# Optimization experiments

Measured on AMD Instinct MI355X. Metric: run time of the kernel, lower is better.

Reference implementation:

```python
import jax, jax.numpy as jnp
import numpy as np

BT, H, V = 4096, 2048, 32000
IGNORE_INDEX = -100


def setup_inputs() -> dict:
    key = jax.random.key(0)
    k1, k2, k3 = jax.random.split(key, 3)
    x = jax.random.normal(k1, (BT, H), dtype=jnp.float32)
    weight = jax.random.normal(k2, (V, H), dtype=jnp.float32) * 0.02
    target = jax.random.randint(k3, (BT,), 0, V, dtype=jnp.int64)
    return {"x": x, "weight": weight, "target": target}


def reference(x, weight, target):
    # logits: [BT, V] = x @ weight.T, accumulated in fp32 (as hl.dot out_dtype)
    logits = jnp.einsum("bh,vh->bv", x, weight).astype(jnp.float32)
    lse = jax.nn.logsumexp(logits, axis=-1)  # [BT]
    # picked target logit (target == ignore_index never matches any class,
    # matching the kernel's mask = (target[:,None] == vocab_offset))
    valid = target != IGNORE_INDEX
    safe_t = jnp.where(valid, target, 0)
    picked = jnp.take_along_axis(logits, safe_t[:, None], axis=-1)[:, 0]
    picked = jnp.where(valid, picked, 0.0)
    nll = lse - picked  # [BT]
    # reduction == 'mean': divide per-token nll by n_non_ignore, then sum
    n_non_ignore = valid.sum().astype(jnp.float32)
    loss = (nll / n_non_ignore).sum()
    return loss
```

## Files before the change

kernel.cpp:

```cpp
#include <hip/hip_runtime.h>
#include <hip/hip_bf16.h>

#define BT 4096
#define HD 2048
#define VD 32000
#define IGNORE_IDX (-100)

#define BM2 256
#define BN2 256
#define BK2 64
#define NRB2 (BT / BM2)
#define NCB2 (VD / BN2)
#define NKT (HD / BK2)

#define BM 128
#define BN 128
#define BKT 32
#define NRB (BT / BM)
#define NCB (VD / BN)

using short8 = __attribute__((ext_vector_type(8))) short;
using f32x4 = __attribute__((ext_vector_type(4))) float;
using i32x4 = __attribute__((ext_vector_type(4))) int;

__device__ __forceinline__ unsigned short f2bf(float f) {
  unsigned u = __float_as_uint(f);
  u = (u + 0x7fffu + ((u >> 16) & 1u)) >> 16;
  return (unsigned short)u;
}

#define GL(SRC, DST)                                         \
  __builtin_amdgcn_global_load_lds(                          \
      (const __attribute__((address_space(1))) void*)(SRC),  \
      (__attribute__((address_space(3))) void*)(DST), 16, 0, 0)

#define STG1(GSRC, KOFF, DBASE, SLOT) GL((GSRC) + (KOFF), (DBASE) + (SLOT)*8192)

__global__ void detect_tgt_kernel(const long long* __restrict__ t64,
                                  int* __restrict__ badcnt) {
  int i = blockIdx.x * blockDim.x + threadIdx.x;
  long long v = t64[i];
  bool valid = (v == (long long)IGNORE_IDX) || (v >= 0 && v < (long long)VD);
  if (!valid) atomicAdd(badcnt, 1);
}

__global__ __launch_bounds__(256) void quant_rows_kernel(
    const float* __restrict__ in, signed char* __restrict__ outq,
    float* __restrict__ scale) {
  const int row = blockIdx.x;
  const int t = threadIdx.x;
  const float* src = in + (size_t)row * HD;
  float4 v0 = ((const float4*)src)[2 * t];
  float4 v1 = ((const float4*)src)[2 * t + 1];
  float vv[8] = {v0.x, v0.y, v0.z, v0.w, v1.x, v1.y, v1.z, v1.w};
  float amax = 0.f;
#pragma unroll
  for (int i = 0; i < 8; i++) amax = fmaxf(amax, fabsf(vv[i]));
#pragma unroll
  for (int m = 1; m < 64; m <<= 1) amax = fmaxf(amax, __shfl_xor(amax, m, 64));
  __shared__ float wm4[4];
  if ((t & 63) == 0) wm4[t >> 6] = amax;
  __syncthreads();
  float am = fmaxf(fmaxf(wm4[0], wm4[1]), fmaxf(wm4[2], wm4[3]));
  float inv = am > 0.f ? 127.f / am : 0.f;
  if (t == 0) scale[row] = am > 0.f ? am / 127.f : 0.f;
  int lo = 0, hi = 0;
#pragma unroll
  for (int i = 0; i < 4; i++) {
    float f = fminf(fmaxf(vv[i] * inv, -127.f), 127.f);
    lo |= (__float2int_rn(f) & 0xff) << (8 * i);
  }
#pragma unroll
  for (int i = 0; i < 4; i++) {
    float f = fminf(fmaxf(vv[4 + i] * inv, -127.f), 127.f);
    hi |= (__float2int_rn(f) & 0xff) << (8 * i);
  }
  int2 pk = make_int2(lo, hi);
  *(int2*)(outq + (size_t)row * HD + t * 8) = pk;
}

__global__ __launch_bounds__(512, 2) void gemm_lse_i8_kernel(
    const signed char* __restrict__ xq, const signed char* __restrict__ wq,
    const float* __restrict__ sx, const float* __restrict__ sw,
    const void* __restrict__ tgt, const int* __restrict__ badcnt,
    float* __restrict__ partialS, float* __restrict__ picked) {
  __shared__ signed char smem[65536];
  signed char* ldsA = smem;
  signed char* ldsB = smem + 32768;

  const int t = threadIdx.x;

  {
    uint4 z = make_uint4(0u, 0u, 0u, 0u);
#pragma unroll
    for (int i = 0; i < 8; i++) ((uint4*)smem)[t + i * 512] = z;
  }
  __syncthreads();

  const int bid = blockIdx.x;
  const int cpx = (NRB2 * NCB2) >> 3;
  const int swz = (bid & 7) * cpx + (bid >> 3);
  const int rb = swz % NRB2;
  const int cb = swz / NRB2;
  const int row0 = rb * BM2;
  const int col0 = cb * BN2;

  const int lane = t & 63;
  const int w = t >> 6;
  const int wm = w >> 2;
  const int wn = w & 3;
  const int bh = wn >> 1;
  const int bn4 = wn & 1;

  const int fr = lane & 15;
  const int kq = lane >> 4;

  const signed char* pA0 = ldsA + (0 * 2 + wm) * 8192 + lane * 16;
  const signed char* pA1 = ldsA + (1 * 2 + wm) * 8192 + lane * 16;
  const signed char* pB0 = ldsB + (0 * 2 + bh) * 8192 + bn4 * 4096 + lane * 16;
  const signed char* pB1 = ldsB + (1 * 2 + bh) * 8192 + bn4 * 4096 + lane * 16;

  const int srow = lane & 15;
  const int scol = (lane >> 4) * 16;
  const signed char* gA0 = xq + (size_t)(row0 + 0 + w * 16 + srow) * HD + scol;
  const signed char* gA1 =
      xq + (size_t)(row0 + 128 + w * 16 + srow) * HD + scol;
  const signed char* gB0 = wq + (size_t)(col0 + 0 + w * 16 + srow) * HD + scol;
  const signed char* gB1 =
      wq + (size_t)(col0 + 128 + w * 16 + srow) * HD + scol;

  signed char* dA = ldsA + w * 1024;
  signed char* dB = ldsB + w * 1024;

  i32x4 acc[8][4];
#pragma unroll
  for (int i = 0; i < 8; i++)
#pragma unroll
    for (int n = 0; n < 4; n++)
#pragma unroll
      for (int q = 0; q < 4; q++) acc[i][n][q] = 0;

  i32x4 aLo[4], aHi[4], bLo[2], bHi[2];

#define RDALO(P)                                       \
  _Pragma("unroll") for (int i = 0; i < 4; i++)        \
      aLo[i] = *(const i32x4*)((P) + i * 1024);

#define RDAHI(P)                                       \
  _Pragma("unroll") for (int i = 0; i < 4; i++)        \
      aHi[i] = *(const i32x4*)((P) + (i + 4) * 1024);

#define RDB(P)                                         \
  _Pragma("unroll") for (int n = 0; n < 2; n++)        \
      bLo[n] = *(const i32x4*)((P) + n * 1024);        \
  _Pragma("unroll") for (int n = 0; n < 2; n++)        \
      bHi[n] = *(const i32x4*)((P) + (n + 2) * 1024);

#define MM_P1()                                                            \
  _Pragma("unroll") for (int i = 0; i < 4; i++) {                          \
    _Pragma("unroll") for (int n = 0; n < 2; n++)                          \
        acc[i][n] = __builtin_amdgcn_mfma_i32_16x16x64_i8(                 \
            aLo[i], bLo[n], acc[i][n], 0, 0, 0);                           \
    _Pragma("unroll") for (int n = 0; n < 2; n++)                          \
        acc[i][2 + n] = __builtin_amdgcn_mfma_i32_16x16x64_i8(             \
            aLo[i], bHi[n], acc[i][2 + n], 0, 0, 0);                       \
  }

#define MM_P2()                                                            \
  _Pragma("unroll") for (int i = 0; i < 4; i++)                            \
  _Pragma("unroll") for (int n = 0; n < 2; n++)                            \
      acc[4 + i][n] = __builtin_amdgcn_mfma_i32_16x16x64_i8(               \
          aHi[i], bLo[n], acc[4 + i][n], 0, 0, 0);

#define MM_P3()                                                            \
  _Pragma("unroll") for (int i = 0; i < 4; i++)                            \
  _Pragma("unroll") for (int n = 0; n < 2; n++)                            \
      acc[4 + i][2 + n] = __builtin_amdgcn_mfma_i32_16x16x64_i8(           \
          aHi[i], bHi[n], acc[4 + i][2 + n], 0, 0, 0);

#define PHASE(BODY)                                    \
  __builtin_amdgcn_sched_barrier(0);                   \
  __builtin_amdgcn_s_barrier();                        \
  asm volatile("s_waitcnt lgkmcnt(0)" ::: "memory");   \
  __builtin_amdgcn_sched_barrier(0);                   \
  __builtin_amdgcn_s_setprio(1);                       \
  BODY();                                              \
  __builtin_amdgcn_s_setprio(0);                       \
  __builtin_amdgcn_sched_barrier(0);                   \
  __builtin_amdgcn_s_barrier();                        \
  __builtin_amdgcn_sched_barrier(0);

  STG1(gA0, 0, dA, 0);
  STG1(gA1, 0, dA, 1);
  STG1(gB0, 0, dB, 0);
  STG1(gB1, 0, dB, 1);
  STG1(gB0, 64, dB, 2);
  STG1(gA0, 64, dA, 2);
  STG1(gA1, 64, dA, 3);
  asm volatile("s_waitcnt vmcnt(3)" ::: "memory");
  __builtin_amdgcn_s_barrier();

  for (int kt = 0; kt + 3 < NKT; kt += 2) {
    RDALO(pA0);
    RDB(pB0);
    STG1(gB1, 64, dB, 3);
    PHASE(MM_P1);
    RDAHI(pA0);
    STG1(gB0, 128, dB, 0);
    PHASE(MM_P2);
    STG1(gA0, 128, dA, 0);
    STG1(gA1, 128, dA, 1);
    asm volatile("s_waitcnt vmcnt(3)" ::: "memory");
    PHASE(MM_P3);
    RDALO(pA1);
    RDB(pB1);
    STG1(gB1, 128, dB, 1);
    PHASE(MM_P1);
    RDAHI(pA1);
    STG1(gB0, 192, dB, 2);
    PHASE(MM_P2);
    STG1(gA0, 192, dA, 2);
    STG1(gA1, 192, dA, 3);
    asm volatile("s_waitcnt vmcnt(3)" ::: "memory");
    PHASE(MM_P3);
    gA0 += 128;
    gA1 += 128;
    gB0 += 128;
    gB1 += 128;
  }

  {
    RDALO(pA0);
    RDB(pB0);
    STG1(gB1, 64, dB, 3);
    PHASE(MM_P1);
    RDAHI(pA0);
    PHASE(MM_P2);
    asm volatile("s_waitcnt vmcnt(0)" ::: "memory");
    PHASE(MM_P3);
    RDALO(pA1);
    RDB(pB1);
    PHASE(MM_P1);
    RDAHI(pA1);
    PHASE(MM_P2);
    PHASE(MM_P3);
  }

  __syncthreads();
  float* sxl = (float*)smem;
  float* swl = ((float*)smem) + 256;
  if (t < 256) {
    sxl[t] = sx[row0 + t];
    swl[t] = sw[col0 + t];
  }
  __syncthreads();
  float* red = ((float*)smem) + 512;
#pragma unroll
  for (int i = 0; i < 8; i++) {
#pragma unroll
    for (int q = 0; q < 4; q++) {
      int lrow = wm * 128 + i * 16 + kq * 4 + q;
      float sxr = sxl[lrow];
      float s = 0.f;
#pragma unroll
      for (int n = 0; n < 4; n++) {
        int lcol = wn * 64 + n * 16 + fr;
        s += __expf((float)acc[i][n][q] * sxr * swl[lcol]);
      }
#pragma unroll
      for (int m = 1; m < 16; m <<= 1) s += __shfl_xor(s, m, 64);
      if (fr == 0) red[lrow * 4 + wn] = s;
    }
  }
  __syncthreads();
  if (t < 256) {
    float S = red[t * 4 + 0] + red[t * 4 + 1] + red[t * 4 + 2] + red[t * 4 + 3];
    partialS[(size_t)cb * BT + row0 + t] = S;
  }

  const bool is64 = (*badcnt == 0);
#pragma unroll
  for (int i = 0; i < 8; i++) {
#pragma unroll
    for (int q = 0; q < 4; q++) {
      int lrow = wm * 128 + i * 16 + kq * 4 + q;
      int grow = row0 + lrow;
      long long tv = is64 ? ((const long long*)tgt)[grow]
                          : (long long)((const int*)tgt)[grow];
#pragma unroll
      for (int n = 0; n < 4; n++) {
        int lcol = wn * 64 + n * 16 + fr;
        int gcol = col0 + lcol;
        if (tv == (long long)gcol)
          picked[grow] = (float)acc[i][n][q] * sxl[lrow] * swl[lcol];
      }
    }
  }
#undef RDALO
#undef RDAHI
#undef RDB
#undef MM_P1
#undef MM_P2
#undef MM_P3
#undef PHASE
}

__global__ __launch_bounds__(256) void gemm_lse_kernel(
    const float* __restrict__ x, const float* __restrict__ w,
    const void* __restrict__ tgt, const int* __restrict__ badcnt,
    float* __restrict__ partialS, float* __restrict__ picked) {
  __shared__ unsigned short As[BM][BKT];
  __shared__ unsigned short Bs[BN][BKT];

  const int bid = blockIdx.x;
  const int rb = bid % NRB;
  const int cb = bid / NRB;
  const int row0 = rb * BM;
  const int col0 = cb * BN;
  const int t = threadIdx.x;
  const int lane = t & 63;
  const int wave = t >> 6;
  const int wr = wave >> 1;
  const int wc = wave & 1;

  const int srow = t >> 3;
  const int scol = (t & 7) * 4;

  const float* xA = x + (size_t)row0 * HD;
  const float* wB = w + (size_t)col0 * HD;

  f32x4 acc[4][4];
#pragma unroll
  for (int i = 0; i < 4; i++)
#pragma unroll
    for (int j = 0; j < 4; j++)
#pragma unroll
      for (int q = 0; q < 4; q++) acc[i][j][q] = 0.f;

  float4 ra[4], rbv[4];

#define STAGE_LOAD(k0)                                                        \
  {                                                                           \
    _Pragma("unroll") for (int j = 0; j < 4; j++) {                           \
      ra[j] = *(const float4*)(xA + (size_t)(srow + j * 32) * HD + (k0) + scol); \
      rbv[j] = *(const float4*)(wB + (size_t)(srow + j * 32) * HD + (k0) + scol); \
    }                                                                         \
  }
#define STAGE_WRITE()                                                         \
  {                                                                           \
    _Pragma("unroll") for (int j = 0; j < 4; j++) {                           \
      ushort4 pa = make_ushort4(f2bf(ra[j].x), f2bf(ra[j].y), f2bf(ra[j].z),  \
                                f2bf(ra[j].w));                               \
      ushort4 pb = make_ushort4(f2bf(rbv[j].x), f2bf(rbv[j].y),               \
                                f2bf(rbv[j].z), f2bf(rbv[j].w));              \
      *(ushort4*)&As[srow + j * 32][scol] = pa;                               \
      *(ushort4*)&Bs[srow + j * 32][scol] = pb;                               \
    }                                                                         \
  }

  const int ks = (lane >> 4) * 8;
  const int fr = lane & 15;

  STAGE_LOAD(0);
  STAGE_WRITE();
  __syncthreads();

  for (int k0 = 0; k0 < HD; k0 += BKT) {
    const bool notlast = (k0 + BKT < HD);
    if (notlast) STAGE_LOAD(k0 + BKT);

    short8 af[4], bfv[4];
#pragma unroll
    for (int i = 0; i < 4; i++) {
      af[i] = *(const short8*)&As[wr * 64 + i * 16 + fr][ks];
      bfv[i] = *(const short8*)&Bs[wc * 64 + i * 16 + fr][ks];
    }
#pragma unroll
    for (int i = 0; i < 4; i++)
#pragma unroll
      for (int j = 0; j < 4; j++)
        acc[i][j] = __builtin_amdgcn_mfma_f32_16x16x32_bf16(af[i], bfv[j],
                                                            acc[i][j], 0, 0, 0);

    __syncthreads();
    if (notlast) STAGE_WRITE();
    __syncthreads();
  }
#undef STAGE_LOAD
#undef STAGE_WRITE

  float rsum[16];
#pragma unroll
  for (int mi = 0; mi < 4; mi++) {
#pragma unroll
    for (int r = 0; r < 4; r++) {
      float s = 0.f;
#pragma unroll
      for (int nj = 0; nj < 4; nj++) s += __expf(acc[mi][nj][r]);
      rsum[mi * 4 + r] = s;
    }
  }
#pragma unroll
  for (int m = 1; m < 16; m <<= 1) {
#pragma unroll
    for (int q = 0; q < 16; q++) rsum[q] += __shfl_xor(rsum[q], m, 64);
  }

  __syncthreads();
  float* red = (float*)&As[0][0];
  if (fr == 0) {
#pragma unroll
    for (int mi = 0; mi < 4; mi++)
#pragma unroll
      for (int r = 0; r < 4; r++)
        red[wave * 64 + mi * 16 + (lane >> 4) * 4 + r] = rsum[mi * 4 + r];
  }
  __syncthreads();

  if (t < BM) {
    int rl = t;
    int wrow = rl >> 6;
    float S = red[(wrow * 2 + 0) * 64 + (rl & 63)] +
              red[(wrow * 2 + 1) * 64 + (rl & 63)];
    partialS[(size_t)cb * BT + row0 + rl] = S;
  }

  const bool is64 = (*badcnt == 0);
#pragma unroll
  for (int mi = 0; mi < 4; mi++) {
#pragma unroll
    for (int r = 0; r < 4; r++) {
      int grow = row0 + wr * 64 + mi * 16 + ((lane >> 4) << 2) + r;
      long long tv = is64 ? ((const long long*)tgt)[grow]
                          : (long long)((const int*)tgt)[grow];
#pragma unroll
      for (int nj = 0; nj < 4; nj++) {
        int gcol = col0 + wc * 64 + nj * 16 + fr;
        if (tv == (long long)gcol) picked[grow] = acc[mi][nj][r];
      }
    }
  }
}

__global__ void reduce_rows_kernel(const float* __restrict__ partialS,
                                   const float* __restrict__ picked,
                                   float* __restrict__ nll, int ncb) {
  int r = blockIdx.x * blockDim.x + threadIdx.x;
  if (r >= BT) return;
  float S = 0.f;
  for (int cb = 0; cb < ncb; cb++) S += partialS[(size_t)cb * BT + r];
  nll[r] = logf(fmaxf(S, 1e-37f)) - picked[r];
}

__global__ void reduce_final_kernel(const float* __restrict__ nll,
                                    const void* __restrict__ tgt,
                                    const int* __restrict__ badcnt,
                                    float* __restrict__ out) {
  __shared__ float ssum[256];
  __shared__ int scnt[256];
  int t = threadIdx.x;
  const bool is64 = (*badcnt == 0);
  float s = 0.f;
  int c = 0;
  for (int r = t; r < BT; r += 256) {
    s += nll[r];
    long long tv =
        is64 ? ((const long long*)tgt)[r] : (long long)((const int*)tgt)[r];
    c += (tv != (long long)IGNORE_IDX) ? 1 : 0;
  }
  ssum[t] = s;
  scnt[t] = c;
  __syncthreads();
  for (int o = 128; o > 0; o >>= 1) {
    if (t < o) {
      ssum[t] += ssum[t + o];
      scnt[t] += scnt[t + o];
    }
    __syncthreads();
  }
  if (t == 0) out[0] = ssum[0] / (float)scnt[0];
}

extern "C" void kernel_launch(void* const* d_in, const int* in_sizes, int n_in,
                              void* d_out, int out_size, void* d_ws,
                              size_t ws_size, hipStream_t stream) {
  const float* x = (const float*)d_in[0];
  const float* w = (const float*)d_in[1];
  const void* tgt = d_in[2];
  float* out = (float*)d_out;

  char* ws = (char*)d_ws;
  const size_t offA = (size_t)NCB * BT * 4;
  float* partialS = (float*)ws;
  int* badcnt = (int*)(ws + offA);
  float* picked = (float*)(ws + offA + 16);
  float* nll = (float*)(ws + offA + 16 + (size_t)BT * 4);
  const size_t offX = offA + 16 + 2 * (size_t)BT * 4;
  const size_t offW = offX + (size_t)BT * HD;
  const size_t offSX = offW + (size_t)VD * HD;
  const size_t offSW = offSX + (size_t)BT * 4;
  const size_t need = offSW + (size_t)VD * 4;

  hipMemsetAsync(ws + offA, 0, 16 + (size_t)BT * 4, stream);

  detect_tgt_kernel<<<8, 256, 0, stream>>>((const long long*)tgt, badcnt);

  if (ws_size >= need) {
    signed char* xq = (signed char*)(ws + offX);
    signed char* wq = (signed char*)(ws + offW);
    float* sx = (float*)(ws + offSX);
    float* sw = (float*)(ws + offSW);
    quant_rows_kernel<<<BT, 256, 0, stream>>>(x, xq, sx);
    quant_rows_kernel<<<VD, 256, 0, stream>>>(w, wq, sw);
    gemm_lse_i8_kernel<<<NRB2 * NCB2, 512, 0, stream>>>(
        xq, wq, sx, sw, tgt, badcnt, partialS, picked);
    reduce_rows_kernel<<<BT / 256, 256, 0, stream>>>(partialS, picked, nll,
                                                     NCB2);
  } else {
    gemm_lse_kernel<<<NRB * NCB, 256, 0, stream>>>(x, w, tgt, badcnt, partialS,
                                                   picked);
    reduce_rows_kernel<<<BT / 256, 256, 0, stream>>>(partialS, picked, nll,
                                                     NCB);
  }

  reduce_final_kernel<<<1, 256, 0, stream>>>(nll, tgt, badcnt, out);
}
```

Measured before the change: 481.2 us.

## Shrink int8 GEMM tile to 128x128 with simpler double-buffered pipeline

Replaces the 256x256-tile, 512-thread int8 GEMM+LSE kernel with a 128x128-tile, 256-thread variant using 32KB LDS, allowing three blocks per CU. The k-loop becomes a plain two-buffer prefetch scheme in place of the three-phase interleaved schedule. The aim is higher occupancy and better wave balance, since 32000 is not divisible by 256. The cost is lower arithmetic intensity per loaded byte, twice as many partial LSE rows for the reduction, and more blocks.

```diff
diff --git a/kernel.cpp b/kernel.cpp
--- a/kernel.cpp
+++ b/kernel.cpp
@@ -6,18 +6,12 @@
 #define VD 32000
 #define IGNORE_IDX (-100)
 
-#define BM2 256
-#define BN2 256
-#define BK2 64
-#define NRB2 (BT / BM2)
-#define NCB2 (VD / BN2)
-#define NKT (HD / BK2)
-
 #define BM 128
 #define BN 128
-#define BKT 32
+#define BK 64
 #define NRB (BT / BM)
 #define NCB (VD / BN)
+#define NKT (HD / BK)
 
 using short8 = __attribute__((ext_vector_type(8))) short;
 using f32x4 = __attribute__((ext_vector_type(4))) float;
@@ -34,7 +28,9 @@
       (const __attribute__((address_space(1))) void*)(SRC),  \
       (__attribute__((address_space(3))) void*)(DST), 16, 0, 0)
 
-#define STG1(GSRC, KOFF, DBASE, SLOT) GL((GSRC) + (KOFF), (DBASE) + (SLOT)*8192)
+#define STG(GSRC, KOFF, DBASE, BUF)                          \
+  GL((GSRC) + (KOFF), (DBASE) + (BUF)*8192);                 \
+  GL((GSRC) + (KOFF) + 16 * HD, (DBASE) + (BUF)*8192 + 1024)
 
 __global__ void detect_tgt_kernel(const long long* __restrict__ t64,
                                   int* __restrict__ badcnt) {
@@ -79,187 +75,134 @@
   *(int2*)(outq + (size_t)row * HD + t * 8) = pk;
 }
 
-__global__ __launch_bounds__(512, 2) void gemm_lse_i8_kernel(
+__global__ __launch_bounds__(256, 3) void gemm_lse_i8_128_kernel(
     const signed char* __restrict__ xq, const signed char* __restrict__ wq,
     const float* __restrict__ sx, const float* __restrict__ sw,
     const void* __restrict__ tgt, const int* __restrict__ badcnt,
     float* __restrict__ partialS, float* __restrict__ picked) {
-  __shared__ signed char smem[65536];
+  __shared__ signed char smem[32768];
   signed char* ldsA = smem;
-  signed char* ldsB = smem + 32768;
+  signed char* ldsB = smem + 16384;
 
   const int t = threadIdx.x;
 
   {
     uint4 z = make_uint4(0u, 0u, 0u, 0u);
 #pragma unroll
-    for (int i = 0; i < 8; i++) ((uint4*)smem)[t + i * 512] = z;
+    for (int i = 0; i < 8; i++) ((uint4*)smem)[t + i * 256] = z;
   }
   __syncthreads();
 
   const int bid = blockIdx.x;
-  const int cpx = (NRB2 * NCB2) >> 3;
+  const int cpx = (NRB * NCB) >> 3;
   const int swz = (bid & 7) * cpx + (bid >> 3);
-  const int rb = swz % NRB2;
-  const int cb = swz / NRB2;
-  const int row0 = rb * BM2;
-  const int col0 = cb * BN2;
+  const int rb = swz % NRB;
+  const int cb = swz / NRB;
+  const int row0 = rb * BM;
+  const int col0 = cb * BN;
 
   const int lane = t & 63;
   const int w = t >> 6;
-  const int wm = w >> 2;
-  const int wn = w & 3;
-  const int bh = wn >> 1;
-  const int bn4 = wn & 1;
+  const int wm = w >> 1;
+  const int wn = w & 1;
 
   const int fr = lane & 15;
   const int kq = lane >> 4;
 
-  const signed char* pA0 = ldsA + (0 * 2 + wm) * 8192 + lane * 16;
-  const signed char* pA1 = ldsA + (1 * 2 + wm) * 8192 + lane * 16;
-  const signed char* pB0 = ldsB + (0 * 2 + bh) * 8192 + bn4 * 4096 + lane * 16;
-  const signed char* pB1 = ldsB + (1 * 2 + bh) * 8192 + bn4 * 4096 + lane * 16;
+  const signed char* pA = ldsA + wm * 4096 + lane * 16;
+  const signed char* pB = ldsB + wn * 4096 + lane * 16;
 
   const int srow = lane & 15;
   const int scol = (lane >> 4) * 16;
-  const signed char* gA0 = xq + (size_t)(row0 + 0 + w * 16 + srow) * HD + scol;
-  const signed char* gA1 =
-      xq + (size_t)(row0 + 128 + w * 16 + srow) * HD + scol;
-  const signed char* gB0 = wq + (size_t)(col0 + 0 + w * 16 + srow) * HD + scol;
-  const signed char* gB1 =
-      wq + (size_t)(col0 + 128 + w * 16 + srow) * HD + scol;
-
-  signed char* dA = ldsA + w * 1024;
-  signed char* dB = ldsB + w * 1024;
-
-  i32x4 acc[8][4];
-#pragma unroll
-  for (int i = 0; i < 8; i++)
+  const signed char* gA = xq + (size_t)(row0 + w * 32 + srow) * HD + scol;
+  const signed char* gB = wq + (size_t)(col0 + w * 32 + srow) * HD + scol;
+
+  signed char* dA = ldsA + w * 2048;
+  signed char* dB = ldsB + w * 2048;
+
+  i32x4 acc[4][4];
+#pragma unroll
+  for (int i = 0; i < 4; i++)
 #pragma unroll
     for (int n = 0; n < 4; n++)
 #pragma unroll
       for (int q = 0; q < 4; q++) acc[i][n][q] = 0;
 
-  i32x4 aLo[4], aHi[4], bLo[2], bHi[2];
-
-#define RDALO(P)                                       \
-  _Pragma("unroll") for (int i = 0; i < 4; i++)        \
-      aLo[i] = *(const i32x4*)((P) + i * 1024);
-
-#define RDAHI(P)                                       \
-  _Pragma("unroll") for (int i = 0; i < 4; i++)        \
-      aHi[i] = *(const i32x4*)((P) + (i + 4) * 1024);
-
-#define RDB(P)                                         \
-  _Pragma("unroll") for (int n = 0; n < 2; n++)        \
-      bLo[n] = *(const i32x4*)((P) + n * 1024);        \
-  _Pragma("unroll") for (int n = 0; n < 2; n++)        \
-      bHi[n] = *(const i32x4*)((P) + (n + 2) * 1024);
-
-#define MM_P1()                                                            \
-  _Pragma("unroll") for (int i = 0; i < 4; i++) {                          \
-    _Pragma("unroll") for (int n = 0; n < 2; n++)                          \
-        acc[i][n] = __builtin_amdgcn_mfma_i32_16x16x64_i8(                 \
-            aLo[i], bLo[n], acc[i][n], 0, 0, 0);                           \
-    _Pragma("unroll") for (int n = 0; n < 2; n++)                          \
-        acc[i][2 + n] = __builtin_amdgcn_mfma_i32_16x16x64_i8(             \
-            aLo[i], bHi[n], acc[i][2 + n], 0, 0, 0);                       \
-  }
-
-#define MM_P2()                                                            \
-  _Pragma("unroll") for (int i = 0; i < 4; i++)                            \
-  _Pragma("unroll") for (int n = 0; n < 2; n++)                            \
-      acc[4 + i][n] = __builtin_amdgcn_mfma_i32_16x16x64_i8(               \
-          aHi[i], bLo[n], acc[4 + i][n], 0, 0, 0);
-
-#define MM_P3()                                                            \
-  _Pragma("unroll") for (int i = 0; i < 4; i++)                            \
-  _Pragma("unroll") for (int n = 0; n < 2; n++)                            \
-      acc[4 + i][2 + n] = __builtin_amdgcn_mfma_i32_16x16x64_i8(           \
-          aHi[i], bHi[n], acc[4 + i][2 + n], 0, 0, 0);
-
-#define PHASE(BODY)                                    \
-  __builtin_amdgcn_sched_barrier(0);                   \
-  __builtin_amdgcn_s_barrier();                        \
-  asm volatile("s_waitcnt lgkmcnt(0)" ::: "memory");   \
-  __builtin_amdgcn_sched_barrier(0);                   \
-  __builtin_amdgcn_s_setprio(1);                       \
-  BODY();                                              \
-  __builtin_amdgcn_s_setprio(0);                       \
-  __builtin_amdgcn_sched_barrier(0);                   \
-  __builtin_amdgcn_s_barrier();                        \
-  __builtin_amdgcn_sched_barrier(0);
-
-  STG1(gA0, 0, dA, 0);
-  STG1(gA1, 0, dA, 1);
-  STG1(gB0, 0, dB, 0);
-  STG1(gB1, 0, dB, 1);
-  STG1(gB0, 64, dB, 2);
-  STG1(gA0, 64, dA, 2);
-  STG1(gA1, 64, dA, 3);
-  asm volatile("s_waitcnt vmcnt(3)" ::: "memory");
+  i32x4 aF[4], bF[4];
+
+#define RD(BUF)                                                      \
+  _Pragma("unroll") for (int i = 0; i < 4; i++)                      \
+      aF[i] = *(const i32x4*)(pA + (BUF)*8192 + i * 1024);           \
+  _Pragma("unroll") for (int n = 0; n < 4; n++)                      \
+      bF[n] = *(const i32x4*)(pB + (BUF)*8192 + n * 1024);
+
+#define MM()                                                         \
+  _Pragma("unroll") for (int i = 0; i < 4; i++)                      \
+  _Pragma("unroll") for (int n = 0; n < 4; n++)                      \
+      acc[i][n] = __builtin_amdgcn_mfma_i32_16x16x64_i8(             \
+          aF[i], bF[n], acc[i][n], 0, 0, 0);
+
+  STG(gA, 0, dA, 0);
+  STG(gB, 0, dB, 0);
+  STG(gA, 64, dA, 1);
+  STG(gB, 64, dB, 1);
+  asm volatile("s_waitcnt vmcnt(4)" ::: "memory");
   __builtin_amdgcn_s_barrier();
 
   for (int kt = 0; kt + 3 < NKT; kt += 2) {
-    RDALO(pA0);
-    RDB(pB0);
-    STG1(gB1, 64, dB, 3);
-    PHASE(MM_P1);
-    RDAHI(pA0);
-    STG1(gB0, 128, dB, 0);
-    PHASE(MM_P2);
-    STG1(gA0, 128, dA, 0);
-    STG1(gA1, 128, dA, 1);
-    asm volatile("s_waitcnt vmcnt(3)" ::: "memory");
-    PHASE(MM_P3);
-    RDALO(pA1);
-    RDB(pB1);
-    STG1(gB1, 128, dB, 1);
-    PHASE(MM_P1);
-    RDAHI(pA1);
-    STG1(gB0, 192, dB, 2);
-    PHASE(MM_P2);
-    STG1(gA0, 192, dA, 2);
-    STG1(gA1, 192, dA, 3);
-    asm volatile("s_waitcnt vmcnt(3)" ::: "memory");
-    PHASE(MM_P3);
-    gA0 += 128;
-    gA1 += 128;
-    gB0 += 128;
-    gB1 += 128;
+    RD(0);
+    asm volatile("s_waitcnt lgkmcnt(0)" ::: "memory");
+    __builtin_amdgcn_s_barrier();
+    STG(gA, 128, dA, 0);
+    STG(gB, 128, dB, 0);
+    __builtin_amdgcn_s_setprio(1);
+    MM();
+    __builtin_amdgcn_s_setprio(0);
+    asm volatile("s_waitcnt vmcnt(4)" ::: "memory");
+    __builtin_amdgcn_s_barrier();
+    RD(1);
+    asm volatile("s_waitcnt lgkmcnt(0)" ::: "memory");
+    __builtin_amdgcn_s_barrier();
+    STG(gA, 192, dA, 1);
+    STG(gB, 192, dB, 1);
+    __builtin_amdgcn_s_setprio(1);
+    MM();
+    __builtin_amdgcn_s_setprio(0);
+    asm volatile("s_waitcnt vmcnt(4)" ::: "memory");
+    __builtin_amdgcn_s_barrier();
+    gA += 128;
+    gB += 128;
   }
 
   {
-    RDALO(pA0);
-    RDB(pB0);
-    STG1(gB1, 64, dB, 3);
-    PHASE(MM_P1);
-    RDAHI(pA0);
-    PHASE(MM_P2);
+    RD(0);
+    asm volatile("s_waitcnt lgkmcnt(0)" ::: "memory");
+    __builtin_amdgcn_s_setprio(1);
+    MM();
+    __builtin_amdgcn_s_setprio(0);
     asm volatile("s_waitcnt vmcnt(0)" ::: "memory");
-    PHASE(MM_P3);
-    RDALO(pA1);
-    RDB(pB1);
-    PHASE(MM_P1);
-    RDAHI(pA1);
-    PHASE(MM_P2);
-    PHASE(MM_P3);
+    __builtin_amdgcn_s_barrier();
+    RD(1);
+    asm volatile("s_waitcnt lgkmcnt(0)" ::: "memory");
+    __builtin_amdgcn_s_setprio(1);
+    MM();
+    __builtin_amdgcn_s_setprio(0);
   }
 
   __syncthreads();
   float* sxl = (float*)smem;
-  float* swl = ((float*)smem) + 256;
-  if (t < 256) {
+  float* swl = sxl + 128;
+  float* red = swl + 128;
+  if (t < 128) {
     sxl[t] = sx[row0 + t];
     swl[t] = sw[col0 + t];
   }
   __syncthreads();
-  float* red = ((float*)smem) + 512;
-#pragma unroll
-  for (int i = 0; i < 8; i++) {
+#pragma unroll
+  for (int i = 0; i < 4; i++) {
 #pragma unroll
     for (int q = 0; q < 4; q++) {
-      int lrow = wm * 128 + i * 16 + kq * 4 + q;
+      int lrow = wm * 64 + i * 16 + kq * 4 + q;
       float sxr = sxl[lrow];
       float s = 0.f;
 #pragma unroll
@@ -269,21 +212,21 @@
       }
 #pragma unroll
       for (int m = 1; m < 16; m <<= 1) s += __shfl_xor(s, m, 64);
-      if (fr == 0) red[lrow * 4 + wn] = s;
-    }
-  }
-  __syncthreads();
-  if (t < 256) {
-    float S = red[t * 4 + 0] + red[t * 4 + 1] + red[t * 4 + 2] + red[t * 4 + 3];
+      if (fr == 0) red[lrow * 2 + wn] = s;
+    }
+  }
+  __syncthreads();
+  if (t < 128) {
+    float S = red[t * 2 + 0] + red[t * 2 + 1];
     partialS[(size_t)cb * BT + row0 + t] = S;
   }
 
   const bool is64 = (*badcnt == 0);
 #pragma unroll
-  for (int i = 0; i < 8; i++) {
+  for (int i = 0; i < 4; i++) {
 #pragma unroll
     for (int q = 0; q < 4; q++) {
-      int lrow = wm * 128 + i * 16 + kq * 4 + q;
+      int lrow = wm * 64 + i * 16 + kq * 4 + q;
       int grow = row0 + lrow;
       long long tv = is64 ? ((const long long*)tgt)[grow]
                           : (long long)((const int*)tgt)[grow];
@@ -296,21 +239,16 @@
       }
     }
   }
-#undef RDALO
-#undef RDAHI
-#undef RDB
-#undef MM_P1
-#undef MM_P2
-#undef MM_P3
-#undef PHASE
+#undef RD
+#undef MM
 }
 
 __global__ __launch_bounds__(256) void gemm_lse_kernel(
     const float* __restrict__ x, const float* __restrict__ w,
     const void* __restrict__ tgt, const int* __restrict__ badcnt,
     float* __restrict__ partialS, float* __restrict__ picked) {
-  __shared__ unsigned short As[BM][BKT];
-  __shared__ unsigned short Bs[BN][BKT];
+  __shared__ unsigned short As[BM][32];
+  __shared__ unsigned short Bs[BN][32];
 
   const int bid = blockIdx.x;
   const int rb = bid % NRB;
@@ -365,9 +303,9 @@
   STAGE_WRITE();
   __syncthreads();
 
-  for (int k0 = 0; k0 < HD; k0 += BKT) {
-    const bool notlast = (k0 + BKT < HD);
-    if (notlast) STAGE_LOAD(k0 + BKT);
+  for (int k0 = 0; k0 < HD; k0 += 32) {
+    const bool notlast = (k0 + 32 < HD);
+    if (notlast) STAGE_LOAD(k0 + 32);
 
     short8 af[4], bfv[4];
 #pragma unroll
@@ -512,10 +450,10 @@
     float* sw = (float*)(ws + offSW);
     quant_rows_kernel<<<BT, 256, 0, stream>>>(x, xq, sx);
     quant_rows_kernel<<<VD, 256, 0, stream>>>(w, wq, sw);
-    gemm_lse_i8_kernel<<<NRB2 * NCB2, 512, 0, stream>>>(
+    gemm_lse_i8_128_kernel<<<NRB * NCB, 256, 0, stream>>>(
         xq, wq, sx, sw, tgt, badcnt, partialS, picked);
     reduce_rows_kernel<<<BT / 256, 256, 0, stream>>>(partialS, picked, nll,
-                                                     NCB2);
+                                                     NCB);
   } else {
     gemm_lse_kernel<<<NRB * NCB, 256, 0, stream>>>(x, w, tgt, badcnt, partialS,
                                                    picked);
```

Result: slower. 667.6 us (+38.7%).
